# Kernel tuning notes

Hardware: AMD Instinct MI355X
Metric: run time of the kernel (lower is better)

Reference implementation:

```python
import jax, jax.numpy as jnp
import numpy as np

NUM_HEADS = 16
KEY_SIZE = 64
MODEL = NUM_HEADS * KEY_SIZE  # 1024
UPPER_FREQ = 10000.0


def _rope_cos_sin(L, dim, dtype):
    inv_freq = 1.0 / (UPPER_FREQ ** (jnp.arange(0, dim, 2, dtype=jnp.float32) / dim))
    t = jnp.arange(L, dtype=jnp.float32)
    freqs = t[:, None] * inv_freq[None, :]            # [L, dim/2]
    cos = jnp.cos(freqs).astype(dtype)[None, :, None, :]  # [1,L,1,dim/2]
    sin = jnp.sin(freqs).astype(dtype)[None, :, None, :]
    return cos, sin


def _apply_rotary(x, cos, sin):
    a, b = x[..., : x.shape[-1] // 2], x[..., x.shape[-1] // 2 :]
    return jnp.concatenate((a * cos - b * sin, b * cos + a * sin), axis=-1)


def setup_inputs() -> dict:
    key = jax.random.key(0)
    ks = jax.random.split(key, 16)
    B, L, D = 2, 2048, MODEL
    s = 0.02
    return {
        "query": jax.random.normal(ks[0], (B, L, D), jnp.float32),
        "key": jax.random.normal(ks[1], (B, L, D), jnp.float32),
        "value": jax.random.normal(ks[2], (B, L, D), jnp.float32),
        "attention_mask": jax.random.randint(ks[3], (B, L, L), 0, 2) > 0,
        "attention_weight_bias": jax.random.normal(ks[4], (1, NUM_HEADS, L, L), jnp.float32),
        "Wq": jax.random.normal(ks[5], (D, D), jnp.float32) * s,
        "bq": jax.random.normal(ks[6], (D,), jnp.float32) * s,
        "Wk": jax.random.normal(ks[7], (D, D), jnp.float32) * s,
        "bk": jax.random.normal(ks[8], (D,), jnp.float32) * s,
        "Wv": jax.random.normal(ks[9], (D, D), jnp.float32) * s,
        "bv": jax.random.normal(ks[10], (D,), jnp.float32) * s,
        "Wo": jax.random.normal(ks[11], (D, D), jnp.float32) * s,
        "bo": jax.random.normal(ks[12], (D,), jnp.float32) * s,
    }


def reference(query, key, value, attention_mask, attention_weight_bias,
              Wq, bq, Wk, bk, Wv, bv, Wo, bo):
    B, L, D = query.shape
    H, Dk = NUM_HEADS, KEY_SIZE
    out_dtype = query.dtype

    q = (query @ Wq.T + bq).reshape(B, L, H, Dk)
    k = (key @ Wk.T + bk).reshape(B, L, H, Dk)
    v = (value @ Wv.T + bv).reshape(B, L, H, Dk)

    cos, sin = _rope_cos_sin(L, Dk, q.dtype)
    q = _apply_rotary(q, cos, sin)
    k = _apply_rotary(k, cos, sin)

    # fp32 attention: [B,H,Lq,Lk]
    logits = jnp.einsum("bqhd,bkhd->bhqk", q.astype(jnp.float32), k.astype(jnp.float32))
    logits = logits / np.sqrt(Dk).astype(np.float32)
    logits = jnp.where(attention_mask[:, None, :, :], logits, jnp.float32(-1e30))
    logits = logits + attention_weight_bias.astype(jnp.float32)
    weights = jax.nn.softmax(logits, axis=-1)

    attn = jnp.einsum("bhqk,bkhd->bqhd", weights, v.astype(jnp.float32))
    attn = attn.astype(out_dtype).reshape(B, L, H * Dk)
    out = attn @ Wo.T + bo
    return out, weights.astype(out_dtype)
```

## Files before the change

kernel.cpp:

```cpp
#include <hip/hip_runtime.h>
#include <cstdint>

typedef _Float16 f16;
typedef _Float16 f16x8 __attribute__((ext_vector_type(8)));
typedef _Float16 f16x4 __attribute__((ext_vector_type(4)));
typedef float f32x4 __attribute__((ext_vector_type(4)));

#define AS1 __attribute__((address_space(1)))
#define AS3 __attribute__((address_space(3)))

#define LSEQ 2048
#define NH 16
#define DKH 64
#define DMOD 1024
#define MROWS 4096

__device__ __forceinline__ void load16_lds(const void* g, void* l) {
  __builtin_amdgcn_global_load_lds((const AS1 uint32_t*)g, (AS3 uint32_t*)l, 16, 0, 0);
}

__global__ __launch_bounds__(256) void cvt_kernel(
    const float* __restrict__ q, const float* __restrict__ k, const float* __restrict__ v,
    const float* __restrict__ wq, const float* __restrict__ wk, const float* __restrict__ wv,
    const float* __restrict__ wo,
    f16* __restrict__ oq, f16* __restrict__ ok, f16* __restrict__ ov,
    f16* __restrict__ owq, f16* __restrict__ owk, f16* __restrict__ owv, f16* __restrict__ owo) {
  const float* src; f16* dst; int n;
  switch (blockIdx.y) {
    case 0: src = q;  dst = oq;  n = MROWS * DMOD; break;
    case 1: src = k;  dst = ok;  n = MROWS * DMOD; break;
    case 2: src = v;  dst = ov;  n = MROWS * DMOD; break;
    case 3: src = wq; dst = owq; n = DMOD * DMOD;  break;
    case 4: src = wk; dst = owk; n = DMOD * DMOD;  break;
    case 5: src = wv; dst = owv; n = DMOD * DMOD;  break;
    default: src = wo; dst = owo; n = DMOD * DMOD; break;
  }
  int i = (blockIdx.x * 256 + threadIdx.x) * 4;
  if (i < n) {
    float4 f = *(const float4*)(src + i);
    f16x4 h = {(f16)f.x, (f16)f.y, (f16)f.z, (f16)f.w};
    *(f16x4*)(dst + i) = h;
  }
}

__global__ __launch_bounds__(256) void maskpack_kernel(const int* __restrict__ mask,
                                                       unsigned long long* __restrict__ bits) {
  int i = blockIdx.x * 256 + threadIdx.x;
  unsigned long long b = __ballot(mask[i] != 0);
  if ((threadIdx.x & 63) == 0) bits[i >> 6] = b;
}

template <typename OutT>
__device__ __forceinline__ void gemm_body(const f16* __restrict__ A, const f16* __restrict__ Bt,
                                          const float* __restrict__ bias, OutT* __restrict__ C) {
  constexpr int K = 1024, NLD = 1024;
  __shared__ __align__(16) f16 As[128 * 32];
  __shared__ __align__(16) f16 Bs[128 * 32];
  const int tid = threadIdx.x, lane = tid & 63, w = tid >> 6;
  const int m0 = blockIdx.x * 128, n0 = blockIdx.y * 128;
  const int wm = (w >> 1) * 64, wn = (w & 1) * 64;
  f32x4 acc[4][4] = {};
  const int e0 = (w * 2 + 0) * 64 + lane;
  const int e1 = (w * 2 + 1) * 64 + lane;
  const f16* ga0 = A + (size_t)(m0 + (e0 >> 2)) * K + (e0 & 3) * 8;
  const f16* ga1 = A + (size_t)(m0 + (e1 >> 2)) * K + (e1 & 3) * 8;
  const f16* gb0 = Bt + (size_t)(n0 + (e0 >> 2)) * K + (e0 & 3) * 8;
  const f16* gb1 = Bt + (size_t)(n0 + (e1 >> 2)) * K + (e1 & 3) * 8;
  f16* lA0 = As + (w * 2 + 0) * 512;
  f16* lA1 = As + (w * 2 + 1) * 512;
  f16* lB0 = Bs + (w * 2 + 0) * 512;
  f16* lB1 = Bs + (w * 2 + 1) * 512;
  for (int kt = 0; kt < K; kt += 32) {
    __syncthreads();
    load16_lds(ga0 + kt, lA0);
    load16_lds(ga1 + kt, lA1);
    load16_lds(gb0 + kt, lB0);
    load16_lds(gb1 + kt, lB1);
    __syncthreads();
    f16x8 af[4], bf[4];
#pragma unroll
    for (int mt = 0; mt < 4; ++mt)
      af[mt] = *(const f16x8*)(As + (wm + mt * 16 + (lane & 15)) * 32 + (lane >> 4) * 8);
#pragma unroll
    for (int nt = 0; nt < 4; ++nt)
      bf[nt] = *(const f16x8*)(Bs + (wn + nt * 16 + (lane & 15)) * 32 + (lane >> 4) * 8);
#pragma unroll
    for (int mt = 0; mt < 4; ++mt)
#pragma unroll
      for (int nt = 0; nt < 4; ++nt)
        acc[mt][nt] = __builtin_amdgcn_mfma_f32_16x16x32_f16(af[mt], bf[nt], acc[mt][nt], 0, 0, 0);
  }
  const int cn = lane & 15, rg = lane >> 4;
#pragma unroll
  for (int nt = 0; nt < 4; ++nt) {
    int n = n0 + wn + nt * 16 + cn;
    float bv = bias[n];
#pragma unroll
    for (int mt = 0; mt < 4; ++mt)
#pragma unroll
      for (int r = 0; r < 4; ++r) {
        int m = m0 + wm + mt * 16 + rg * 4 + r;
        C[(size_t)m * NLD + n] = (OutT)(acc[mt][nt][r] + bv);
      }
  }
}

__global__ __launch_bounds__(256) void gemm_qkv_kernel(
    const f16* A0, const f16* A1, const f16* A2,
    const f16* B0, const f16* B1, const f16* B2,
    const float* c0, const float* c1, const float* c2,
    f16* O0, f16* O1, f16* O2) {
  const f16* A; const f16* Bt; const float* bias; f16* O;
  if (blockIdx.z == 0)      { A = A0; Bt = B0; bias = c0; O = O0; }
  else if (blockIdx.z == 1) { A = A1; Bt = B1; bias = c1; O = O1; }
  else                      { A = A2; Bt = B2; bias = c2; O = O2; }
  gemm_body<f16>(A, Bt, bias, O);
}

__global__ __launch_bounds__(256) void gemm_out_kernel(const f16* __restrict__ A,
                                                       const f16* __restrict__ Bt,
                                                       const float* __restrict__ bias,
                                                       float* __restrict__ C) {
  gemm_body<float>(A, Bt, bias, C);
}

__global__ __launch_bounds__(256) void rope_kernel(const f16* __restrict__ qin, const f16* __restrict__ kin,
                                                   f16* __restrict__ qout, f16* __restrict__ kout) {
  int t = blockIdx.x * 256 + threadIdx.x;
  int i = t & 31;
  int h = (t >> 5) & 15;
  int l = (t >> 9) & 2047;
  int b = t >> 20;
  const f16* src = (blockIdx.y == 0) ? qin : kin;
  f16* dst = (blockIdx.y == 0) ? qout : kout;
  size_t inb = (((size_t)(b * 2048 + l)) * 16 + h) * 64;
  float a = (float)src[inb + i];
  float c2 = (float)src[inb + 32 + i];
  float invf = powf(10000.0f, -(float)i * (1.0f / 32.0f));
  float fr = (float)l * invf;
  float cs = cosf(fr), sn = sinf(fr);
  size_t outb = (((size_t)(b * 16 + h)) * 2048 + l) * 64;
  dst[outb + i]      = (f16)(a * cs - c2 * sn);
  dst[outb + 32 + i] = (f16)(c2 * cs + a * sn);
}

__global__ __launch_bounds__(256) void vtrans_kernel(const f16* __restrict__ vin, f16* __restrict__ vout) {
  __shared__ f16 tile[64][72];
  int bh = blockIdx.y;
  int b = bh >> 4, h = bh & 15;
  int l0 = blockIdx.x * 64;
  int t = threadIdx.x;
#pragma unroll
  for (int j = 0; j < 16; ++j) {
    int e = t + 256 * j;
    int l = e >> 6, d = e & 63;
    tile[d][l] = vin[(((size_t)(b * 2048 + l0 + l)) * 16 + h) * 64 + d];
  }
  __syncthreads();
#pragma unroll
  for (int j = 0; j < 16; ++j) {
    int e = t + 256 * j;
    int d = e >> 6, l = e & 63;
    vout[((size_t)(b * 16 + h) * 64 + d) * 2048 + l0 + l] = tile[d][l];
  }
}

#define ATTN_LDS (65536 + 512)
__global__ __launch_bounds__(256, 2) void attn_kernel(
    const f16* __restrict__ qr, const f16* __restrict__ kr, const f16* __restrict__ vt,
    const float* __restrict__ bias, const unsigned int* __restrict__ mbits,
    float* __restrict__ wout, f16* __restrict__ attnout) {
  extern __shared__ char smem[];
  f16* S = (f16*)smem;
  float* red = (float*)(smem + 65536);

  int bid = blockIdx.x;
  int b = bid & 1, qt = (bid >> 1) & 127, h = bid >> 8;
  int q0 = qt * 16;
  int tid = threadIdx.x, lane = tid & 63, w = tid >> 6;

  const f16* Qp = qr + (((size_t)(b * 16 + h)) * 2048 + q0) * 64;
  const f16* Kp = kr + ((size_t)(b * 16 + h)) * 2048 * 64;
  const f16* Vp = vt + ((size_t)(b * 16 + h)) * 64 * 2048;
  const float* brow = bias + ((size_t)h * 2048 + q0) * 2048;
  const unsigned int* mrow = mbits + ((size_t)(b * 2048 + q0)) * 64;
  float* Wrow = wout + (((size_t)(b * 16 + h)) * 2048 + q0) * 2048;

  const int qi = lane & 15, kg = lane >> 4;
  f16x8 qf0 = *(const f16x8*)(Qp + qi * 64 + kg * 8);
  f16x8 qf1 = *(const f16x8*)(Qp + qi * 64 + kg * 8 + 32);

  float lmax = -3.0e38f;
#pragma unroll 2
  for (int nt = 0; nt < 32; ++nt) {
    int k0 = w * 512 + nt * 16;
    f16x8 a0 = *(const f16x8*)(Kp + (size_t)(k0 + qi) * 64 + kg * 8);
    f16x8 a1 = *(const f16x8*)(Kp + (size_t)(k0 + qi) * 64 + kg * 8 + 32);
    f32x4 acc = {0.f, 0.f, 0.f, 0.f};
    acc = __builtin_amdgcn_mfma_f32_16x16x32_f16(a0, qf0, acc, 0, 0, 0);
    acc = __builtin_amdgcn_mfma_f32_16x16x32_f16(a1, qf1, acc, 0, 0, 0);
    int kk = k0 + kg * 4;
    float4 b4 = *(const float4*)(brow + (size_t)qi * 2048 + kk);
    unsigned int mword = mrow[qi * 64 + (kk >> 5)];
    float v0, v1, v2, v3;
    v0 = ((mword >> ((kk & 31) + 0)) & 1u) ? acc[0] * 0.125f + b4.x : -30000.0f;
    v1 = ((mword >> ((kk & 31) + 1)) & 1u) ? acc[1] * 0.125f + b4.y : -30000.0f;
    v2 = ((mword >> ((kk & 31) + 2)) & 1u) ? acc[2] * 0.125f + b4.z : -30000.0f;
    v3 = ((mword >> ((kk & 31) + 3)) & 1u) ? acc[3] * 0.125f + b4.w : -30000.0f;
    lmax = fmaxf(fmaxf(lmax, fmaxf(v0, v1)), fmaxf(v2, v3));
    f16x4 hv = {(f16)v0, (f16)v1, (f16)v2, (f16)v3};
    *(f16x4*)(S + (kk >> 3) * 128 + qi * 8 + (kk & 4)) = hv;
  }
  lmax = fmaxf(lmax, __shfl_xor(lmax, 16, 64));
  lmax = fmaxf(lmax, __shfl_xor(lmax, 32, 64));
  if (lane < 16) red[w * 16 + lane] = lmax;
  __syncthreads();

  const int q2 = tid & 15, c2 = tid >> 4;
  float m = fmaxf(fmaxf(red[q2], red[16 + q2]), fmaxf(red[32 + q2], red[48 + q2]));
  float psum = 0.f;
#pragma unroll 4
  for (int i = 0; i < 16; ++i) {
    int chunk = c2 + (i << 4);
    f16x8 hv = *(const f16x8*)(S + chunk * 128 + q2 * 8);
#pragma unroll
    for (int j = 0; j < 8; ++j) psum += __expf((float)hv[j] - m);
  }
  psum += __shfl_xor(psum, 16, 64);
  psum += __shfl_xor(psum, 32, 64);
  if (lane < 16) red[64 + w * 16 + lane] = psum;
  __syncthreads();
  float denom = red[64 + q2] + red[80 + q2] + red[96 + q2] + red[112 + q2];
  float rinv = 1.0f / denom;

#pragma unroll 2
  for (int i = 0; i < 16; ++i) {
    int chunk = c2 + (i << 4);
    f16* sp = S + chunk * 128 + q2 * 8;
    f16x8 hv = *(const f16x8*)sp;
    float e0 = __expf((float)hv[0] - m) * rinv;
    float e1 = __expf((float)hv[1] - m) * rinv;
    float e2 = __expf((float)hv[2] - m) * rinv;
    float e3 = __expf((float)hv[3] - m) * rinv;
    float e4 = __expf((float)hv[4] - m) * rinv;
    float e5 = __expf((float)hv[5] - m) * rinv;
    float e6 = __expf((float)hv[6] - m) * rinv;
    float e7 = __expf((float)hv[7] - m) * rinv;
    float4 o0 = {e0, e1, e2, e3};
    float4 o1 = {e4, e5, e6, e7};
    *(float4*)(Wrow + (size_t)q2 * 2048 + chunk * 8) = o0;
    *(float4*)(Wrow + (size_t)q2 * 2048 + chunk * 8 + 4) = o1;
    f16x8 he = {(f16)e0, (f16)e1, (f16)e2, (f16)e3, (f16)e4, (f16)e5, (f16)e6, (f16)e7};
    *(f16x8*)sp = he;
  }
  __syncthreads();

  f32x4 oacc[4] = {};
#pragma unroll 4
  for (int kt = 0; kt < 16; ++kt) {
    int kbase = w * 512 + kt * 32;
    f16x8 af = *(const f16x8*)(S + ((kbase + kg * 8) >> 3) * 128 + qi * 8);
#pragma unroll
    for (int nt = 0; nt < 4; ++nt) {
      f16x8 bv = *(const f16x8*)(Vp + (size_t)(nt * 16 + qi) * 2048 + kbase + kg * 8);
      oacc[nt] = __builtin_amdgcn_mfma_f32_16x16x32_f16(af, bv, oacc[nt], 0, 0, 0);
    }
  }
  __syncthreads();
  float* Ob = (float*)smem;
#pragma unroll
  for (int nt = 0; nt < 4; ++nt)
#pragma unroll
    for (int r = 0; r < 4; ++r)
      Ob[(w * 16 + kg * 4 + r) * 68 + nt * 16 + qi] = oacc[nt][r];
  __syncthreads();
  int qv = tid >> 4, d0 = (tid & 15) * 4;
  float sx = 0.f, sy = 0.f, sz = 0.f, sw = 0.f;
#pragma unroll
  for (int w4 = 0; w4 < 4; ++w4) {
    const float* p = &Ob[(w4 * 16 + qv) * 68 + d0];
    sx += p[0]; sy += p[1]; sz += p[2]; sw += p[3];
  }
  f16x4 hs = {(f16)sx, (f16)sy, (f16)sz, (f16)sw};
  *(f16x4*)(attnout + ((size_t)(b * 2048 + q0 + qv)) * 1024 + h * 64 + d0) = hs;
}

extern "C" void kernel_launch(void* const* d_in, const int* in_sizes, int n_in,
                              void* d_out, int out_size, void* d_ws, size_t ws_size,
                              hipStream_t stream) {
  const float* q    = (const float*)d_in[0];
  const float* k    = (const float*)d_in[1];
  const float* v    = (const float*)d_in[2];
  const int*   mask = (const int*)d_in[3];
  const float* bias = (const float*)d_in[4];
  const float* Wq = (const float*)d_in[5];  const float* bq = (const float*)d_in[6];
  const float* Wk = (const float*)d_in[7];  const float* bk = (const float*)d_in[8];
  const float* Wv = (const float*)d_in[9];  const float* bv = (const float*)d_in[10];
  const float* Wo = (const float*)d_in[11]; const float* bo = (const float*)d_in[12];
  float* out  = (float*)d_out;
  float* wout = out + (size_t)MROWS * DMOD;

  char* ws = (char*)d_ws;
  const size_t MB = 1u << 20;
  f16* qf   = (f16*)(ws + 0 * MB);
  f16* kf   = (f16*)(ws + 8 * MB);
  f16* vf   = (f16*)(ws + 16 * MB);
  f16* wq16 = (f16*)(ws + 24 * MB);
  f16* wk16 = (f16*)(ws + 26 * MB);
  f16* wv16 = (f16*)(ws + 28 * MB);
  f16* wo16 = (f16*)(ws + 30 * MB);
  f16* qhat = (f16*)(ws + 32 * MB);
  f16* khat = (f16*)(ws + 40 * MB);
  f16* vhat = (f16*)(ws + 48 * MB);
  unsigned long long* mbits = (unsigned long long*)(ws + 56 * MB);
  f16* qrot = qf; f16* krot = kf; f16* vtr = vf; f16* attnf = qhat;

  dim3 blk(256);
  cvt_kernel<<<dim3(4096, 7), blk, 0, stream>>>(q, k, v, Wq, Wk, Wv, Wo,
                                                qf, kf, vf, wq16, wk16, wv16, wo16);
  maskpack_kernel<<<dim3(32768), blk, 0, stream>>>(mask, mbits);
  gemm_qkv_kernel<<<dim3(32, 8, 3), blk, 0, stream>>>(qf, kf, vf, wq16, wk16, wv16,
                                                      bq, bk, bv, qhat, khat, vhat);
  rope_kernel<<<dim3(8192, 2), blk, 0, stream>>>(qhat, khat, qrot, krot);
  vtrans_kernel<<<dim3(32, 32), blk, 0, stream>>>(vhat, vtr);
  (void)hipFuncSetAttribute((const void*)attn_kernel,
                            hipFuncAttributeMaxDynamicSharedMemorySize, ATTN_LDS);
  attn_kernel<<<dim3(4096), blk, ATTN_LDS, stream>>>(qrot, krot, vtr, bias,
                                                     (const unsigned int*)mbits, wout, attnf);
  gemm_out_kernel<<<dim3(32, 8, 1), blk, 0, stream>>>(attnf, wo16, bo, out);
}
```

Measured before the change: 1.247 ms.

## Halve attention query tile to 8 rows to cut LDS and raise occupancy

The attention kernel now handles 8 query rows per block instead of 16. This halves the score buffer in LDS to 32KB of static shared memory and lets launch bounds allow 4 blocks per CU, with twice as many blocks launched. The MFMA still computes 16 query columns, so half of each QK^T tile is wasted compute and every K/V tile is loaded twice as often across blocks. The aim is more parallelism and better latency hiding for the bias-read and weights-write memory traffic.

```diff
diff --git a/kernel.cpp b/kernel.cpp
--- a/kernel.cpp
+++ b/kernel.cpp
@@ -165,18 +165,16 @@
   }
 }
 
-#define ATTN_LDS (65536 + 512)
-__global__ __launch_bounds__(256, 2) void attn_kernel(
+__global__ __launch_bounds__(256, 4) void attn_kernel(
     const f16* __restrict__ qr, const f16* __restrict__ kr, const f16* __restrict__ vt,
     const float* __restrict__ bias, const unsigned int* __restrict__ mbits,
     float* __restrict__ wout, f16* __restrict__ attnout) {
-  extern __shared__ char smem[];
-  f16* S = (f16*)smem;
-  float* red = (float*)(smem + 65536);
+  __shared__ __align__(16) f16 S[256 * 64];
+  __shared__ float red[64];
 
   int bid = blockIdx.x;
-  int b = bid & 1, qt = (bid >> 1) & 127, h = bid >> 8;
-  int q0 = qt * 16;
+  int b = bid & 1, qt = (bid >> 1) & 255, h = bid >> 9;
+  int q0 = qt * 8;
   int tid = threadIdx.x, lane = tid & 63, w = tid >> 6;
 
   const f16* Qp = qr + (((size_t)(b * 16 + h)) * 2048 + q0) * 64;
@@ -187,56 +185,60 @@
   float* Wrow = wout + (((size_t)(b * 16 + h)) * 2048 + q0) * 2048;
 
   const int qi = lane & 15, kg = lane >> 4;
-  f16x8 qf0 = *(const f16x8*)(Qp + qi * 64 + kg * 8);
-  f16x8 qf1 = *(const f16x8*)(Qp + qi * 64 + kg * 8 + 32);
+  const int qq = qi & 7;
+  f16x8 qf0 = *(const f16x8*)(Qp + qq * 64 + kg * 8);
+  f16x8 qf1 = *(const f16x8*)(Qp + qq * 64 + kg * 8 + 32);
 
   float lmax = -3.0e38f;
-#pragma unroll 2
-  for (int nt = 0; nt < 32; ++nt) {
-    int k0 = w * 512 + nt * 16;
-    f16x8 a0 = *(const f16x8*)(Kp + (size_t)(k0 + qi) * 64 + kg * 8);
-    f16x8 a1 = *(const f16x8*)(Kp + (size_t)(k0 + qi) * 64 + kg * 8 + 32);
-    f32x4 acc = {0.f, 0.f, 0.f, 0.f};
-    acc = __builtin_amdgcn_mfma_f32_16x16x32_f16(a0, qf0, acc, 0, 0, 0);
-    acc = __builtin_amdgcn_mfma_f32_16x16x32_f16(a1, qf1, acc, 0, 0, 0);
-    int kk = k0 + kg * 4;
-    float4 b4 = *(const float4*)(brow + (size_t)qi * 2048 + kk);
-    unsigned int mword = mrow[qi * 64 + (kk >> 5)];
-    float v0, v1, v2, v3;
-    v0 = ((mword >> ((kk & 31) + 0)) & 1u) ? acc[0] * 0.125f + b4.x : -30000.0f;
-    v1 = ((mword >> ((kk & 31) + 1)) & 1u) ? acc[1] * 0.125f + b4.y : -30000.0f;
-    v2 = ((mword >> ((kk & 31) + 2)) & 1u) ? acc[2] * 0.125f + b4.z : -30000.0f;
-    v3 = ((mword >> ((kk & 31) + 3)) & 1u) ? acc[3] * 0.125f + b4.w : -30000.0f;
-    lmax = fmaxf(fmaxf(lmax, fmaxf(v0, v1)), fmaxf(v2, v3));
-    f16x4 hv = {(f16)v0, (f16)v1, (f16)v2, (f16)v3};
-    *(f16x4*)(S + (kk >> 3) * 128 + qi * 8 + (kk & 4)) = hv;
-  }
+  for (int it = 0; it < 32; ++it) {
+    int k0 = w * 512 + it * 16;
+    f16x8 alo = *(const f16x8*)(Kp + (size_t)(k0 + qi) * 64 + kg * 8);
+    f16x8 ahi = *(const f16x8*)(Kp + (size_t)(k0 + qi) * 64 + kg * 8 + 32);
+    f32x4 a = {0.f, 0.f, 0.f, 0.f};
+    a = __builtin_amdgcn_mfma_f32_16x16x32_f16(alo, qf0, a, 0, 0, 0);
+    a = __builtin_amdgcn_mfma_f32_16x16x32_f16(ahi, qf1, a, 0, 0, 0);
+    if (qi < 8) {
+      int kk = k0 + kg * 4;
+      float4 b4 = *(const float4*)(brow + (size_t)qi * 2048 + kk);
+      unsigned int mword = mrow[qi * 64 + (kk >> 5)];
+      float v0, v1, v2, v3;
+      v0 = ((mword >> ((kk & 31) + 0)) & 1u) ? a[0] * 0.125f + b4.x : -30000.0f;
+      v1 = ((mword >> ((kk & 31) + 1)) & 1u) ? a[1] * 0.125f + b4.y : -30000.0f;
+      v2 = ((mword >> ((kk & 31) + 2)) & 1u) ? a[2] * 0.125f + b4.z : -30000.0f;
+      v3 = ((mword >> ((kk & 31) + 3)) & 1u) ? a[3] * 0.125f + b4.w : -30000.0f;
+      lmax = fmaxf(fmaxf(lmax, fmaxf(v0, v1)), fmaxf(v2, v3));
+      f16x4 hv = {(f16)v0, (f16)v1, (f16)v2, (f16)v3};
+      *(f16x4*)(S + (kk >> 3) * 64 + qi * 8 + (kk & 4)) = hv;
+    }
+  }
+  lmax = fmaxf(lmax, __shfl_xor(lmax, 8, 64));
   lmax = fmaxf(lmax, __shfl_xor(lmax, 16, 64));
   lmax = fmaxf(lmax, __shfl_xor(lmax, 32, 64));
-  if (lane < 16) red[w * 16 + lane] = lmax;
-  __syncthreads();
-
-  const int q2 = tid & 15, c2 = tid >> 4;
-  float m = fmaxf(fmaxf(red[q2], red[16 + q2]), fmaxf(red[32 + q2], red[48 + q2]));
+  if (lane < 8) red[w * 8 + lane] = lmax;
+  __syncthreads();
+
+  const int q2 = tid & 7, c2 = tid >> 3;
+  float m = fmaxf(fmaxf(red[q2], red[8 + q2]), fmaxf(red[16 + q2], red[24 + q2]));
   float psum = 0.f;
-#pragma unroll 4
-  for (int i = 0; i < 16; ++i) {
-    int chunk = c2 + (i << 4);
-    f16x8 hv = *(const f16x8*)(S + chunk * 128 + q2 * 8);
+#pragma unroll
+  for (int i = 0; i < 8; ++i) {
+    int chunk = c2 + (i << 5);
+    f16x8 hv = *(const f16x8*)(S + chunk * 64 + q2 * 8);
 #pragma unroll
     for (int j = 0; j < 8; ++j) psum += __expf((float)hv[j] - m);
   }
+  psum += __shfl_xor(psum, 8, 64);
   psum += __shfl_xor(psum, 16, 64);
   psum += __shfl_xor(psum, 32, 64);
-  if (lane < 16) red[64 + w * 16 + lane] = psum;
-  __syncthreads();
-  float denom = red[64 + q2] + red[80 + q2] + red[96 + q2] + red[112 + q2];
+  if (lane < 8) red[32 + w * 8 + lane] = psum;
+  __syncthreads();
+  float denom = red[32 + q2] + red[40 + q2] + red[48 + q2] + red[56 + q2];
   float rinv = 1.0f / denom;
 
 #pragma unroll 2
-  for (int i = 0; i < 16; ++i) {
-    int chunk = c2 + (i << 4);
-    f16* sp = S + chunk * 128 + q2 * 8;
+  for (int i = 0; i < 8; ++i) {
+    int chunk = c2 + (i << 5);
+    f16* sp = S + chunk * 64 + q2 * 8;
     f16x8 hv = *(const f16x8*)sp;
     float e0 = __expf((float)hv[0] - m) * rinv;
     float e1 = __expf((float)hv[1] - m) * rinv;
@@ -259,7 +261,7 @@
 #pragma unroll 4
   for (int kt = 0; kt < 16; ++kt) {
     int kbase = w * 512 + kt * 32;
-    f16x8 af = *(const f16x8*)(S + ((kbase + kg * 8) >> 3) * 128 + qi * 8);
+    f16x8 af = *(const f16x8*)(S + ((kbase >> 3) + kg) * 64 + qq * 8);
 #pragma unroll
     for (int nt = 0; nt < 4; ++nt) {
       f16x8 bv = *(const f16x8*)(Vp + (size_t)(nt * 16 + qi) * 2048 + kbase + kg * 8);
@@ -267,22 +269,23 @@
     }
   }
   __syncthreads();
-  float* Ob = (float*)smem;
-#pragma unroll
-  for (int nt = 0; nt < 4; ++nt)
-#pragma unroll
-    for (int r = 0; r < 4; ++r)
-      Ob[(w * 16 + kg * 4 + r) * 68 + nt * 16 + qi] = oacc[nt][r];
-  __syncthreads();
-  int qv = tid >> 4, d0 = (tid & 15) * 4;
-  float sx = 0.f, sy = 0.f, sz = 0.f, sw = 0.f;
-#pragma unroll
-  for (int w4 = 0; w4 < 4; ++w4) {
-    const float* p = &Ob[(w4 * 16 + qv) * 68 + d0];
-    sx += p[0]; sy += p[1]; sz += p[2]; sw += p[3];
-  }
-  f16x4 hs = {(f16)sx, (f16)sy, (f16)sz, (f16)sw};
-  *(f16x4*)(attnout + ((size_t)(b * 2048 + q0 + qv)) * 1024 + h * 64 + d0) = hs;
+  float* Ob = (float*)S;
+  if (kg < 2) {
+#pragma unroll
+    for (int nt = 0; nt < 4; ++nt)
+#pragma unroll
+      for (int r = 0; r < 4; ++r)
+        Ob[(w * 8 + kg * 4 + r) * 68 + nt * 16 + qi] = oacc[nt][r];
+  }
+  __syncthreads();
+#pragma unroll
+  for (int r2 = 0; r2 < 2; ++r2) {
+    int q = w * 2 + r2;
+    float s = 0.f;
+#pragma unroll
+    for (int w4 = 0; w4 < 4; ++w4) s += Ob[(w4 * 8 + q) * 68 + lane];
+    attnout[((size_t)(b * 2048 + q0 + q)) * 1024 + h * 64 + lane] = (f16)s;
+  }
 }
 
 extern "C" void kernel_launch(void* const* d_in, const int* in_sizes, int n_in,
@@ -323,9 +326,7 @@
                                                       bq, bk, bv, qhat, khat, vhat);
   rope_kernel<<<dim3(8192, 2), blk, 0, stream>>>(qhat, khat, qrot, krot);
   vtrans_kernel<<<dim3(32, 32), blk, 0, stream>>>(vhat, vtr);
-  (void)hipFuncSetAttribute((const void*)attn_kernel,
-                            hipFuncAttributeMaxDynamicSharedMemorySize, ATTN_LDS);
-  attn_kernel<<<dim3(4096), blk, ATTN_LDS, stream>>>(qrot, krot, vtr, bias,
-                                                     (const unsigned int*)mbits, wout, attnf);
+  attn_kernel<<<dim3(8192), blk, 0, stream>>>(qrot, krot, vtr, bias,
+                                              (const unsigned int*)mbits, wout, attnf);
   gemm_out_kernel<<<dim3(32, 8, 1), blk, 0, stream>>>(attnf, wo16, bo, out);
 }
```

Result: slower. 1.386 ms (+11.2%).

## Move mask/bias into row-owned softmax pass with swizzled LDS and shuffle reductions

Applied to the files above, without the earlier changes.

The QK^T loop now stores only scaled logits into LDS, using an XOR swizzle on the query index. Bias and mask are applied in a second pass where each group of 16 threads owns one query row and reads contiguous 32-byte bias chunks. Because each row now sits inside one wavefront, the max and sum reductions use intra-wave shuffles, which removes the LDS reduction buffer and two block barriers. In exchange the logits make an extra fp16 round trip through LDS before the bias is added, which adds one more LDS read/write pass and a small precision change.

```diff
diff --git a/kernel.cpp b/kernel.cpp
--- a/kernel.cpp
+++ b/kernel.cpp
@@ -165,14 +165,13 @@
   }
 }
 
-#define ATTN_LDS (65536 + 512)
+#define ATTN_LDS 65536
 __global__ __launch_bounds__(256, 2) void attn_kernel(
     const f16* __restrict__ qr, const f16* __restrict__ kr, const f16* __restrict__ vt,
     const float* __restrict__ bias, const unsigned int* __restrict__ mbits,
     float* __restrict__ wout, f16* __restrict__ attnout) {
   extern __shared__ char smem[];
   f16* S = (f16*)smem;
-  float* red = (float*)(smem + 65536);
 
   int bid = blockIdx.x;
   int b = bid & 1, qt = (bid >> 1) & 127, h = bid >> 8;
@@ -190,66 +189,89 @@
   f16x8 qf0 = *(const f16x8*)(Qp + qi * 64 + kg * 8);
   f16x8 qf1 = *(const f16x8*)(Qp + qi * 64 + kg * 8 + 32);
 
-  float lmax = -3.0e38f;
 #pragma unroll 2
-  for (int nt = 0; nt < 32; ++nt) {
-    int k0 = w * 512 + nt * 16;
-    f16x8 a0 = *(const f16x8*)(Kp + (size_t)(k0 + qi) * 64 + kg * 8);
-    f16x8 a1 = *(const f16x8*)(Kp + (size_t)(k0 + qi) * 64 + kg * 8 + 32);
-    f32x4 acc = {0.f, 0.f, 0.f, 0.f};
-    acc = __builtin_amdgcn_mfma_f32_16x16x32_f16(a0, qf0, acc, 0, 0, 0);
-    acc = __builtin_amdgcn_mfma_f32_16x16x32_f16(a1, qf1, acc, 0, 0, 0);
+  for (int it = 0; it < 32; ++it) {
+    int k0 = w * 512 + it * 16;
+    f16x8 alo = *(const f16x8*)(Kp + (size_t)(k0 + qi) * 64 + kg * 8);
+    f16x8 ahi = *(const f16x8*)(Kp + (size_t)(k0 + qi) * 64 + kg * 8 + 32);
+    f32x4 a = {0.f, 0.f, 0.f, 0.f};
+    a = __builtin_amdgcn_mfma_f32_16x16x32_f16(alo, qf0, a, 0, 0, 0);
+    a = __builtin_amdgcn_mfma_f32_16x16x32_f16(ahi, qf1, a, 0, 0, 0);
     int kk = k0 + kg * 4;
-    float4 b4 = *(const float4*)(brow + (size_t)qi * 2048 + kk);
-    unsigned int mword = mrow[qi * 64 + (kk >> 5)];
-    float v0, v1, v2, v3;
-    v0 = ((mword >> ((kk & 31) + 0)) & 1u) ? acc[0] * 0.125f + b4.x : -30000.0f;
-    v1 = ((mword >> ((kk & 31) + 1)) & 1u) ? acc[1] * 0.125f + b4.y : -30000.0f;
-    v2 = ((mword >> ((kk & 31) + 2)) & 1u) ? acc[2] * 0.125f + b4.z : -30000.0f;
-    v3 = ((mword >> ((kk & 31) + 3)) & 1u) ? acc[3] * 0.125f + b4.w : -30000.0f;
-    lmax = fmaxf(fmaxf(lmax, fmaxf(v0, v1)), fmaxf(v2, v3));
-    f16x4 hv = {(f16)v0, (f16)v1, (f16)v2, (f16)v3};
-    *(f16x4*)(S + (kk >> 3) * 128 + qi * 8 + (kk & 4)) = hv;
-  }
-  lmax = fmaxf(lmax, __shfl_xor(lmax, 16, 64));
-  lmax = fmaxf(lmax, __shfl_xor(lmax, 32, 64));
-  if (lane < 16) red[w * 16 + lane] = lmax;
-  __syncthreads();
-
-  const int q2 = tid & 15, c2 = tid >> 4;
-  float m = fmaxf(fmaxf(red[q2], red[16 + q2]), fmaxf(red[32 + q2], red[48 + q2]));
+    int ch = kk >> 3;
+    f16x4 hv = {(f16)(a[0] * 0.125f), (f16)(a[1] * 0.125f),
+                (f16)(a[2] * 0.125f), (f16)(a[3] * 0.125f)};
+    *(f16x4*)(S + ch * 128 + ((qi ^ (ch & 7)) * 8) + (kk & 4)) = hv;
+  }
+  __syncthreads();
+
+  const int q = tid >> 4, j = tid & 15;
+  const float* bq = brow + (size_t)q * 2048;
+  const unsigned int* mq = mrow + q * 64;
+  float* Wq_ = Wrow + (size_t)q * 2048;
+
+  float vmax = -3.0e38f;
+#pragma unroll 4
+  for (int i = 0; i < 16; ++i) {
+    int c = j + i * 16;
+    f16* sp = S + c * 128 + ((q ^ (c & 7)) * 8);
+    float4 b0 = *(const float4*)(bq + c * 8);
+    float4 b1 = *(const float4*)(bq + c * 8 + 4);
+    unsigned int mb = mq[c >> 2] >> ((c & 3) * 8);
+    f16x8 s8 = *(const f16x8*)sp;
+    float v0 = (mb & 1u)   ? (float)s8[0] + b0.x : -30000.0f;
+    float v1 = (mb & 2u)   ? (float)s8[1] + b0.y : -30000.0f;
+    float v2 = (mb & 4u)   ? (float)s8[2] + b0.z : -30000.0f;
+    float v3 = (mb & 8u)   ? (float)s8[3] + b0.w : -30000.0f;
+    float v4 = (mb & 16u)  ? (float)s8[4] + b1.x : -30000.0f;
+    float v5 = (mb & 32u)  ? (float)s8[5] + b1.y : -30000.0f;
+    float v6 = (mb & 64u)  ? (float)s8[6] + b1.z : -30000.0f;
+    float v7 = (mb & 128u) ? (float)s8[7] + b1.w : -30000.0f;
+    vmax = fmaxf(vmax, fmaxf(fmaxf(fmaxf(v0, v1), fmaxf(v2, v3)),
+                             fmaxf(fmaxf(v4, v5), fmaxf(v6, v7))));
+    f16x8 hv = {(f16)v0, (f16)v1, (f16)v2, (f16)v3, (f16)v4, (f16)v5, (f16)v6, (f16)v7};
+    *(f16x8*)sp = hv;
+  }
+  vmax = fmaxf(vmax, __shfl_xor(vmax, 1, 64));
+  vmax = fmaxf(vmax, __shfl_xor(vmax, 2, 64));
+  vmax = fmaxf(vmax, __shfl_xor(vmax, 4, 64));
+  vmax = fmaxf(vmax, __shfl_xor(vmax, 8, 64));
+  const float m = vmax;
+
   float psum = 0.f;
 #pragma unroll 4
   for (int i = 0; i < 16; ++i) {
-    int chunk = c2 + (i << 4);
-    f16x8 hv = *(const f16x8*)(S + chunk * 128 + q2 * 8);
-#pragma unroll
-    for (int j = 0; j < 8; ++j) psum += __expf((float)hv[j] - m);
-  }
-  psum += __shfl_xor(psum, 16, 64);
-  psum += __shfl_xor(psum, 32, 64);
-  if (lane < 16) red[64 + w * 16 + lane] = psum;
-  __syncthreads();
-  float denom = red[64 + q2] + red[80 + q2] + red[96 + q2] + red[112 + q2];
-  float rinv = 1.0f / denom;
+    int c = j + i * 16;
+    const f16* sp = S + c * 128 + ((q ^ (c & 7)) * 8);
+    f16x8 v8 = *(const f16x8*)sp;
+    psum += __expf((float)v8[0] - m) + __expf((float)v8[1] - m) +
+            __expf((float)v8[2] - m) + __expf((float)v8[3] - m) +
+            __expf((float)v8[4] - m) + __expf((float)v8[5] - m) +
+            __expf((float)v8[6] - m) + __expf((float)v8[7] - m);
+  }
+  psum += __shfl_xor(psum, 1, 64);
+  psum += __shfl_xor(psum, 2, 64);
+  psum += __shfl_xor(psum, 4, 64);
+  psum += __shfl_xor(psum, 8, 64);
+  const float rinv = 1.0f / psum;
 
 #pragma unroll 2
   for (int i = 0; i < 16; ++i) {
-    int chunk = c2 + (i << 4);
-    f16* sp = S + chunk * 128 + q2 * 8;
-    f16x8 hv = *(const f16x8*)sp;
-    float e0 = __expf((float)hv[0] - m) * rinv;
-    float e1 = __expf((float)hv[1] - m) * rinv;
-    float e2 = __expf((float)hv[2] - m) * rinv;
-    float e3 = __expf((float)hv[3] - m) * rinv;
-    float e4 = __expf((float)hv[4] - m) * rinv;
-    float e5 = __expf((float)hv[5] - m) * rinv;
-    float e6 = __expf((float)hv[6] - m) * rinv;
-    float e7 = __expf((float)hv[7] - m) * rinv;
+    int c = j + i * 16;
+    f16* sp = S + c * 128 + ((q ^ (c & 7)) * 8);
+    f16x8 v8 = *(const f16x8*)sp;
+    float e0 = __expf((float)v8[0] - m) * rinv;
+    float e1 = __expf((float)v8[1] - m) * rinv;
+    float e2 = __expf((float)v8[2] - m) * rinv;
+    float e3 = __expf((float)v8[3] - m) * rinv;
+    float e4 = __expf((float)v8[4] - m) * rinv;
+    float e5 = __expf((float)v8[5] - m) * rinv;
+    float e6 = __expf((float)v8[6] - m) * rinv;
+    float e7 = __expf((float)v8[7] - m) * rinv;
     float4 o0 = {e0, e1, e2, e3};
     float4 o1 = {e4, e5, e6, e7};
-    *(float4*)(Wrow + (size_t)q2 * 2048 + chunk * 8) = o0;
-    *(float4*)(Wrow + (size_t)q2 * 2048 + chunk * 8 + 4) = o1;
+    *(float4*)(Wq_ + c * 8) = o0;
+    *(float4*)(Wq_ + c * 8 + 4) = o1;
     f16x8 he = {(f16)e0, (f16)e1, (f16)e2, (f16)e3, (f16)e4, (f16)e5, (f16)e6, (f16)e7};
     *(f16x8*)sp = he;
   }
@@ -259,7 +281,8 @@
 #pragma unroll 4
   for (int kt = 0; kt < 16; ++kt) {
     int kbase = w * 512 + kt * 32;
-    f16x8 af = *(const f16x8*)(S + ((kbase + kg * 8) >> 3) * 128 + qi * 8);
+    int ch = (kbase >> 3) + kg;
+    f16x8 af = *(const f16x8*)(S + ch * 128 + ((qi ^ (ch & 7)) * 8));
 #pragma unroll
     for (int nt = 0; nt < 4; ++nt) {
       f16x8 bv = *(const f16x8*)(Vp + (size_t)(nt * 16 + qi) * 2048 + kbase + kg * 8);
```

Measured after the change: 1.192 ms. -4.3%, faster.
